# Optimization experiments

Measured on AMD Instinct MI355X. Metric: run time of the kernel, lower is better.

The kernel has to match this reference:

```python
import jax, jax.numpy as jnp
import numpy as np

P = 0.7
WALKS_PER_NODE = 1
WALK_LENGTH = 3


def setup_inputs() -> dict:
    key = jax.random.key(0)
    N = 1_000_000
    E = 16_000_000
    k1, k2 = jax.random.split(key)
    row = jax.random.randint(k1, (E,), 0, N)
    col = jax.random.randint(k2, (E,), 0, N)
    edge_index = jnp.stack([row, col])  # [2, E]
    return {"edge_index": edge_index, "num_nodes": N}


def reference(edge_index, num_nodes):
    E = edge_index.shape[1]
    row, col = edge_index[0], edge_index[1]

    # sort_edge_index: lexicographic sort by (row, col) via two stable argsorts
    p1 = jnp.argsort(col, stable=True)
    p2 = jnp.argsort(row[p1], stable=True)
    perm = p1[p2]
    row, col = row[perm], col[perm]

    # CSR rowptr from out-degree
    deg = jax.ops.segment_sum(jnp.ones(E, jnp.int32), row, num_segments=num_nodes)
    rowptr = jnp.concatenate([jnp.zeros(1, deg.dtype), jnp.cumsum(deg)])

    # start nodes: random permutation, take round(N*p), repeat walks_per_node times
    num_start = int(round(num_nodes * P))
    kperm, kwalk = jax.random.split(jax.random.key(42))
    start = jax.random.permutation(kperm, num_nodes)[:num_start]
    start = jnp.tile(start, WALKS_PER_NODE)  # [S]

    def step(carry, k):
        cur, active = carry
        d = deg[cur]                                  # [S] degree of current node
        act = active & (d > 0)                        # walkers with neighbors
        u = jax.random.uniform(k, cur.shape)
        off = jnp.floor(u * d.astype(u.dtype)).astype(cur.dtype)
        off = jnp.minimum(off, jnp.maximum(d - 1, 0).astype(cur.dtype))
        nxt = col[rowptr[cur] + off]                  # random neighbor gather
        # NOTE: faithful to source, e_id records current_node (used as an
        # index into the edge mask, as the original code does)
        eid = cur
        cur = jnp.where(act, nxt, cur)
        return (cur, act), (eid, act)

    keys = jax.random.split(kwalk, WALK_LENGTH)
    init = (start, jnp.ones(start.shape, bool))
    _, (e_ids, valids) = jax.lax.scan(step, init, keys)

    e_flat = e_ids.reshape(-1)
    v_flat = valids.reshape(-1)
    # scatter hits; invalid entries routed out-of-bounds and dropped
    hits = jnp.zeros(E, bool).at[jnp.where(v_flat, e_flat, E)].set(True, mode='drop')
    edge_mask = ~hits

    # fixed-shape compaction of edge_index[:, edge_mask] / edge_index[:, ~edge_mask]
    ei = jnp.stack([row, col])                        # sorted edge_index [2, E]
    order_keep = jnp.argsort(~edge_mask, stable=True)
    order_mask = jnp.argsort(edge_mask, stable=True)
    n_keep = edge_mask.sum()
    ar = jnp.arange(E)
    remaining_edges = jnp.where(ar < n_keep, ei[:, order_keep], -1)
    masked_edges = jnp.where(ar < (E - n_keep), ei[:, order_mask], -1)
    return remaining_edges, masked_edges, edge_mask
```

## Files before the change

### kernel.cpp

```cpp
#include <hip/hip_runtime.h>
#include <stdint.h>

#define THREADS 256
#define ITEMS 16
#define CHUNK (THREADS * ITEMS)
#define COLMASK 0xFFFFFu
#define EDIG 4096
#define BR 256
#define BCAP 4608
#define BPHYS (BCAP + (BCAP >> 5) + 8)
#define PDIG 1024

__host__ __device__ static inline void tf2x32(uint32_t k0, uint32_t k1,
                                              uint32_t x0, uint32_t x1,
                                              uint32_t* o0, uint32_t* o1) {
  uint32_t ks[3] = {k0, k1, k0 ^ k1 ^ 0x1BD11BDAu};
  x0 += ks[0]; x1 += ks[1];
  const uint32_t RA[4] = {13u, 15u, 26u, 6u};
  const uint32_t RB[4] = {17u, 29u, 16u, 24u};
#pragma unroll
  for (int g = 0; g < 5; ++g) {
    const uint32_t* R = (g & 1) ? RB : RA;
#pragma unroll
    for (int j = 0; j < 4; ++j) {
      x0 += x1;
      x1 = (x1 << R[j]) | (x1 >> (32u - R[j]));
      x1 ^= x0;
    }
    x0 += ks[(g + 1) % 3];
    x1 += ks[(g + 2) % 3] + (uint32_t)(g + 1);
  }
  *o0 = x0; *o1 = x1;
}

__device__ static inline uint32_t rbits32(uint32_t ka, uint32_t kb, uint32_t i) {
  uint32_t o0, o1;
  tf2x32(ka, kb, 0u, i, &o0, &o1);
  return o0 ^ o1;
}

__device__ static inline int xcd_swz(int orig, int nwg) {
  int q = nwg >> 3, r = nwg & 7;
  int xcd = orig & 7, idx = orig >> 3;
  return (xcd < r ? xcd * (q + 1) : r * (q + 1) + (xcd - r) * q) + idx;
}

__device__ static inline int swz32(int j) { return j + (j >> 5); }

__device__ static inline uint32_t block_scan_excl(uint32_t v, uint32_t* lds) {
  int t = threadIdx.x;
  lds[t] = v;
  __syncthreads();
#pragma unroll
  for (int d = 1; d < THREADS; d <<= 1) {
    uint32_t add = (t >= d) ? lds[t - d] : 0u;
    __syncthreads();
    lds[t] += add;
    __syncthreads();
  }
  return lds[t] - v;
}

__global__ void k_sums_u32(const uint32_t* __restrict__ d, int n, uint32_t* __restrict__ bsums) {
  __shared__ uint32_t lds[THREADS];
  int b = blockIdx.x, t = threadIdx.x;
  int base = b * CHUNK + t * ITEMS;
  uint32_t s = 0;
#pragma unroll
  for (int j = 0; j < ITEMS; ++j) { int i = base + j; if (i < n) s += d[i]; }
  lds[t] = s; __syncthreads();
  for (int d2 = THREADS / 2; d2 > 0; d2 >>= 1) { if (t < d2) lds[t] += lds[t + d2]; __syncthreads(); }
  if (t == 0) bsums[b] = lds[0];
}

__global__ void k_scan_single(uint32_t* __restrict__ d, int n, uint32_t* __restrict__ total_out) {
  __shared__ uint32_t lds[THREADS];
  int t = threadIdx.x;
  int K = (n + THREADS - 1) / THREADS;
  int s0 = t * K, s1 = (s0 + K < n) ? (s0 + K) : n;
  uint32_t s = 0;
  for (int j = s0; j < s1; ++j) s += d[j];
  lds[t] = s; __syncthreads();
#pragma unroll
  for (int dd = 1; dd < THREADS; dd <<= 1) {
    uint32_t a = (t >= dd) ? lds[t - dd] : 0u;
    __syncthreads();
    lds[t] += a;
    __syncthreads();
  }
  uint32_t incl = lds[t];
  if (total_out && t == THREADS - 1) *total_out = incl;
  uint32_t run = incl - s;
  for (int j = s0; j < s1; ++j) { uint32_t tmp = d[j]; d[j] = run; run += tmp; }
}

__global__ void k_excl_u32(uint32_t* __restrict__ d, int n, const uint32_t* __restrict__ bsums) {
  __shared__ uint32_t lds[THREADS];
  int b = blockIdx.x, t = threadIdx.x;
  int base = b * CHUNK + t * ITEMS;
  uint32_t v[ITEMS]; uint32_t s = 0;
#pragma unroll
  for (int j = 0; j < ITEMS; ++j) { int i = base + j; uint32_t x = (i < n) ? d[i] : 0u; v[j] = x; s += x; }
  uint32_t run = bsums[b] + block_scan_excl(s, lds);
#pragma unroll
  for (int j = 0; j < ITEMS; ++j) { int i = base + j; if (i < n) d[i] = run; run += v[j]; }
}

__global__ void k_dig_starts(const uint32_t* __restrict__ hist, int NB, int DIG, int total,
                             uint32_t* __restrict__ dstart) {
  int d = blockIdx.x * blockDim.x + threadIdx.x;
  if (d < DIG) dstart[d] = hist[(size_t)d * NB];
  else if (d == DIG) dstart[DIG] = (uint32_t)total;
}

__global__ void k_hist12(const int* __restrict__ row, int n, int NB, uint32_t* __restrict__ hist) {
  __shared__ uint32_t h[EDIG];
  int b = blockIdx.x, t = threadIdx.x;
#pragma unroll
  for (int g = 0; g < EDIG / THREADS; ++g) h[g * THREADS + t] = 0;
  __syncthreads();
  int base = b * CHUNK;
  for (int j = t; j < CHUNK; j += THREADS) {
    int i = base + j;
    if (i < n) atomicAdd(&h[((uint32_t)row[i]) >> 8], 1u);
  }
  __syncthreads();
#pragma unroll
  for (int g = 0; g < EDIG / THREADS; ++g) {
    int d = g * THREADS + t;
    hist[(size_t)d * NB + b] = h[d];
  }
}

__global__ __launch_bounds__(THREADS) void k_pack_scatter12(
    const int* __restrict__ row, const int* __restrict__ col,
    uint64_t* __restrict__ kout, const uint32_t* __restrict__ hist, int n, int NB) {
  constexpr int G = EDIG / THREADS;
  __shared__ uint64_t lkeys[CHUNK];
  __shared__ uint32_t cur[EDIG];
  int b = xcd_swz(blockIdx.x, gridDim.x), t = threadIdx.x;
  int base = b * CHUNK;
#pragma unroll
  for (int g = 0; g < G; ++g) cur[g * THREADS + t] = 0;
  __syncthreads();
  uint64_t mykey[ITEMS];
#pragma unroll
  for (int batch = 0; batch < ITEMS; ++batch) {
    int i = base + batch * THREADS + t;
    uint64_t key = 0ull;
    if (i < n) {
      uint32_t r = (uint32_t)row[i];
      key = ((uint64_t)r << 20) | (uint32_t)col[i];
      atomicAdd(&cur[r >> 8], 1u);
    }
    mykey[batch] = key;
  }
  __syncthreads();
  uint32_t c[G], go[G], lstv[G];
  uint32_t s = 0;
#pragma unroll
  for (int g = 0; g < G; ++g) { c[g] = cur[G * t + g]; s += c[g]; }
  uint32_t tp = block_scan_excl(s, (uint32_t*)lkeys);
  __syncthreads();
#pragma unroll
  for (int g = 0; g < G; ++g) {
    int d = G * t + g;
    go[g] = hist[(size_t)d * NB + b];
    lstv[g] = tp;
    cur[d] = tp;
    tp += c[g];
  }
  __syncthreads();
#pragma unroll
  for (int batch = 0; batch < ITEMS; ++batch) {
    int i = base + batch * THREADS + t;
    if (i < n) {
      uint64_t key = mykey[batch];
      uint32_t dig = (uint32_t)(key >> 28);
      uint32_t slot = atomicAdd(&cur[dig], 1u);
      lkeys[slot] = key;
    }
  }
  __syncthreads();
#pragma unroll
  for (int g = 0; g < G; ++g) cur[G * t + g] = go[g] - lstv[g];
  __syncthreads();
  int nloc = n - base; if (nloc > CHUNK) nloc = CHUNK;
  for (int j = t; j < nloc; j += THREADS) {
    uint64_t key = lkeys[j];
    uint32_t dig = (uint32_t)(key >> 28);
    kout[cur[dig] + (uint32_t)j] = key;
  }
}

__global__ __launch_bounds__(THREADS) void k_bucket256(
    const uint64_t* __restrict__ U0, uint64_t* __restrict__ U1,
    const uint32_t* __restrict__ dstart, int E, int Nn, int* __restrict__ rowptr) {
  __shared__ uint32_t lbuf[BPHYS];
  __shared__ uint8_t  rowof[BCAP];
  __shared__ uint32_t cnt[BR];
  __shared__ uint32_t bs[BR + 1];
  int b = blockIdx.x, t = threadIdx.x;
  int s = (int)dstart[b];
  int e = (int)dstart[b + 1];
  int nseg = e - s;
  int r0 = b * BR;
  cnt[t] = 0;
  __syncthreads();
  for (int j = t; j < nseg; j += THREADS)
    atomicAdd(&cnt[(uint32_t)(U0[s + j] >> 20) & (BR - 1)], 1u);
  __syncthreads();
  uint32_t myc = cnt[t];
  uint32_t mybase = block_scan_excl(myc, lbuf);
  __syncthreads();
  bs[t] = mybase;
  if (t == THREADS - 1) bs[BR] = mybase + myc;
  cnt[t] = mybase;
  __syncthreads();
  if (nseg <= BCAP) {
    for (int j = t; j < nseg; j += THREADS) {
      uint64_t key = U0[s + j];
      uint32_t rl = (uint32_t)(key >> 20) & (BR - 1);
      uint32_t slot = atomicAdd(&cnt[rl], 1u);
      lbuf[swz32((int)slot)] = (uint32_t)(key & COLMASK);
      rowof[slot] = (uint8_t)rl;
    }
    __syncthreads();
    {
      int a0 = (int)bs[t], a1 = (int)bs[t + 1];
      for (int a = a0 + 1; a < a1; ++a) {
        uint32_t key = lbuf[swz32(a)];
        int p = a - 1;
        while (p >= a0 && lbuf[swz32(p)] > key) { lbuf[swz32(p + 1)] = lbuf[swz32(p)]; --p; }
        lbuf[swz32(p + 1)] = key;
      }
    }
    __syncthreads();
    for (int j = t; j < nseg; j += THREADS) {
      uint64_t key = ((uint64_t)(uint32_t)(r0 + rowof[j]) << 20) | lbuf[swz32(j)];
      U1[s + j] = key;
    }
  } else {
    for (int j = t; j < nseg; j += THREADS) {
      uint64_t key = U0[s + j];
      uint32_t slot = atomicAdd(&cnt[(uint32_t)(key >> 20) & (BR - 1)], 1u);
      U1[s + slot] = key;
    }
    __syncthreads();
    int a0 = s + (int)bs[t], a1 = s + (int)bs[t + 1];
    for (int a = a0 + 1; a < a1; ++a) {
      uint64_t key = U1[a];
      int p = a - 1;
      while (p >= a0 && U1[p] > key) { U1[p + 1] = U1[p]; --p; }
      U1[p + 1] = key;
    }
  }
  int r = r0 + t;
  if (r < Nn) rowptr[r] = s + (int)bs[t];
  if (b == (int)gridDim.x - 1 && t == 0) rowptr[Nn] = E;
}

__global__ void k_genkeys64(uint32_t ka, uint32_t kb, int n, uint64_t* __restrict__ K,
                            int NB, uint32_t* __restrict__ hist) {
  __shared__ uint32_t h[PDIG];
  int b = blockIdx.x, t = threadIdx.x;
#pragma unroll
  for (int g = 0; g < PDIG / THREADS; ++g) h[g * THREADS + t] = 0;
  __syncthreads();
  int base = b * CHUNK;
  for (int j = t; j < CHUNK; j += THREADS) {
    int i = base + j;
    if (i < n) {
      uint32_t rb = rbits32(ka, kb, (uint32_t)i);
      K[i] = ((uint64_t)rb << 20) | (uint32_t)i;
      atomicAdd(&h[rb >> 22], 1u);
    }
  }
  __syncthreads();
#pragma unroll
  for (int g = 0; g < PDIG / THREADS; ++g) {
    int d = g * THREADS + t;
    hist[(size_t)d * NB + b] = h[d];
  }
}

__global__ __launch_bounds__(THREADS) void k_scatter64p(
    const uint64_t* __restrict__ kin, uint64_t* __restrict__ kout,
    const uint32_t* __restrict__ hist, int n, int NB) {
  constexpr int G = PDIG / THREADS;
  __shared__ uint64_t lkeys[CHUNK];
  __shared__ uint32_t cur[PDIG];
  int b = blockIdx.x, t = threadIdx.x;
  int base = b * CHUNK;
#pragma unroll
  for (int g = 0; g < G; ++g) cur[g * THREADS + t] = 0;
  __syncthreads();
  uint64_t mykey[ITEMS];
#pragma unroll
  for (int batch = 0; batch < ITEMS; ++batch) {
    int i = base + batch * THREADS + t;
    uint64_t key = 0ull;
    if (i < n) {
      key = kin[i];
      atomicAdd(&cur[(uint32_t)(key >> 42)], 1u);
    }
    mykey[batch] = key;
  }
  __syncthreads();
  uint32_t c[G], go[G], lstv[G];
  uint32_t s = 0;
#pragma unroll
  for (int g = 0; g < G; ++g) { c[g] = cur[G * t + g]; s += c[g]; }
  uint32_t tp = block_scan_excl(s, (uint32_t*)lkeys);
  __syncthreads();
#pragma unroll
  for (int g = 0; g < G; ++g) {
    int d = G * t + g;
    go[g] = hist[(size_t)d * NB + b];
    lstv[g] = tp;
    cur[d] = tp;
    tp += c[g];
  }
  __syncthreads();
#pragma unroll
  for (int batch = 0; batch < ITEMS; ++batch) {
    int i = base + batch * THREADS + t;
    if (i < n) {
      uint64_t key = mykey[batch];
      uint32_t dig = (uint32_t)(key >> 42);
      uint32_t slot = atomicAdd(&cur[dig], 1u);
      lkeys[slot] = key;
    }
  }
  __syncthreads();
#pragma unroll
  for (int g = 0; g < G; ++g) cur[G * t + g] = go[g] - lstv[g];
  __syncthreads();
  int nloc = n - base; if (nloc > CHUNK) nloc = CHUNK;
  for (int j = t; j < nloc; j += THREADS) {
    uint64_t key = lkeys[j];
    uint32_t dig = (uint32_t)(key >> 42);
    kout[cur[dig] + (uint32_t)j] = key;
  }
}

__global__ __launch_bounds__(THREADS) void k_psort(
    const uint64_t* __restrict__ K, const uint32_t* __restrict__ dstart,
    uint32_t* __restrict__ outv, const uint32_t* __restrict__ gsrc) {
  __shared__ uint64_t sb[2048];
  int b = blockIdx.x, t = threadIdx.x;
  int s = (int)dstart[b], e = (int)dstart[b + 1];
  int nseg = e - s;
  for (int j = t; j < 2048; j += THREADS)
    sb[j] = (j < nseg) ? K[s + j] : ~0ull;
  __syncthreads();
  for (int k = 2; k <= 2048; k <<= 1) {
    for (int j = k >> 1; j > 0; j >>= 1) {
      for (int i = t; i < 2048; i += THREADS) {
        int l = i ^ j;
        if (l > i) {
          bool up = ((i & k) == 0);
          uint64_t a = sb[i], c = sb[l];
          if ((a > c) == up) { sb[i] = c; sb[l] = a; }
        }
      }
      __syncthreads();
    }
  }
  for (int j = t; j < nseg; j += THREADS) {
    uint32_t p = (uint32_t)(sb[j] & COLMASK);
    outv[s + j] = gsrc ? gsrc[p] : p;
  }
}

__global__ void k_walk(const int* __restrict__ start, int S,
                       const int* __restrict__ rowptr, const uint64_t* __restrict__ U,
                       uint8_t* __restrict__ hits,
                       uint32_t k0a, uint32_t k0b, uint32_t k1a, uint32_t k1b,
                       uint32_t k2a, uint32_t k2b) {
  int i = blockIdx.x * blockDim.x + threadIdx.x;
  int st = gridDim.x * blockDim.x;
  for (; i < S; i += st) {
    int cur = start[i];
    bool active = true;
    uint32_t ka[3] = {k0a, k1a, k2a};
    uint32_t kb[3] = {k0b, k1b, k2b};
#pragma unroll
    for (int s = 0; s < 3; ++s) {
      int rp = rowptr[cur];
      int d = rowptr[cur + 1] - rp;
      bool act = active && (d > 0);
      if (act) hits[cur] = 1;
      uint32_t bits = rbits32(ka[s], kb[s], (uint32_t)i);
      float u = __uint_as_float((bits >> 9) | 0x3f800000u) - 1.0f;
      int off = (int)floorf(u * (float)d);
      int dm1 = d - 1; if (dm1 < 0) dm1 = 0;
      if (off > dm1) off = dm1;
      if (act) cur = (int)(U[rp + off] & COLMASK);
      active = act;
    }
  }
}

__global__ void k_mask_copy(const uint8_t* __restrict__ hits, const uint64_t* __restrict__ U,
                            int Nn, uint32_t* __restrict__ bsums, uint64_t* __restrict__ hstage) {
  __shared__ uint32_t lds[THREADS];
  int b = blockIdx.x, t = threadIdx.x;
  int base = b * CHUNK + t * ITEMS;
  uint32_t s = 0;
#pragma unroll
  for (int j = 0; j < ITEMS; ++j) {
    int i = base + j;
    if (i < Nn) { s += (uint32_t)(!hits[i]); hstage[i] = U[i]; }
  }
  lds[t] = s; __syncthreads();
  for (int d2 = THREADS / 2; d2 > 0; d2 >>= 1) { if (t < d2) lds[t] += lds[t + d2]; __syncthreads(); }
  if (t == 0) bsums[b] = lds[0];
}

__global__ void k_out_tail(const uint64_t* __restrict__ U, int E, int Nn,
                           const uint32_t* __restrict__ keephead,
                           int* __restrict__ A, int* __restrict__ B, int* __restrict__ M) {
  int nm = Nn - (int)*keephead;
  int i = Nn + blockIdx.x * blockDim.x + threadIdx.x;
  int st = gridDim.x * blockDim.x;
  for (; i < E; i += st) {
    uint64_t key = U[i];
    A[i - nm] = (int)(key >> 20);
    B[i - nm] = (int)(key & COLMASK);
    M[i] = 1;
  }
}

__global__ void k_out_headCD(const uint64_t* __restrict__ hstage, const uint8_t* __restrict__ hits,
                             int Nn, const uint32_t* __restrict__ bsums,
                             int* __restrict__ A, int* __restrict__ B,
                             int* __restrict__ C, int* __restrict__ D, int* __restrict__ M) {
  __shared__ uint32_t lds[THREADS];
  int b = blockIdx.x, t = threadIdx.x;
  int base = b * CHUNK + t * ITEMS;
  uint32_t keep[ITEMS]; uint32_t s = 0;
#pragma unroll
  for (int j = 0; j < ITEMS; ++j) {
    int i = base + j;
    uint32_t k = (i < Nn) ? (uint32_t)(!hits[i]) : 0u;
    keep[j] = k; s += k;
  }
  uint32_t kr = bsums[b] + block_scan_excl(s, lds);
#pragma unroll
  for (int j = 0; j < ITEMS; ++j) {
    int i = base + j;
    if (i < Nn) {
      uint64_t key = hstage[i];
      if (keep[j]) { A[kr] = (int)(key >> 20); B[kr] = (int)(key & COLMASK); M[i] = 1; ++kr; }
      else { uint32_t mr = (uint32_t)i - kr; C[mr] = (int)(key >> 20); D[mr] = (int)(key & COLMASK); M[i] = 0; }
    }
  }
}

__global__ void k_cdfill(int E, int Nn, const uint32_t* __restrict__ keephead,
                         int* __restrict__ A, int* __restrict__ B,
                         int* __restrict__ C, int* __restrict__ D) {
  int nm = Nn - (int)*keephead;
  int j = blockIdx.x * blockDim.x + threadIdx.x;
  int st = gridDim.x * blockDim.x;
  for (; j < E; j += st) {
    if (j >= nm) { C[j] = -1; D[j] = -1; }
    if (j >= E - nm) { A[j] = -1; B[j] = -1; }
  }
}

extern "C" void kernel_launch(void* const* d_in, const int* in_sizes, int n_in,
                              void* d_out, int out_size, void* d_ws, size_t ws_size,
                              hipStream_t stream) {
  const int E = in_sizes[0] / 2;
  const int Nn = 1000000;
  const int S = 700000;
  const int NB_N = (Nn + CHUNK - 1) / CHUNK;
  const int NB_E = (E + CHUNK - 1) / CHUNK;
  const int NBUCK = (Nn + BR - 1) / BR;
  const int NB_P = (Nn + CHUNK - 1) / CHUNK;

  const int* row = (const int*)d_in[0];
  const int* col = row + (size_t)E;

  int* out = (int*)d_out;
  int* A = out;
  int* B = out + (size_t)E;
  int* C = out + (size_t)2 * E;
  int* D = out + (size_t)3 * E;
  int* M = out + (size_t)4 * E;
  uint64_t* U0 = (uint64_t*)out;
  uint64_t* U1 = (uint64_t*)(out + (size_t)2 * E);
  uint32_t* ehist = (uint32_t*)U1;

  char* w = (char*)d_ws;
  uint64_t* hstage = (uint64_t*)w;
  int* rowptr = (int*)w;
  w += (size_t)Nn * 8;
  uint8_t* hits = (uint8_t*)w; w += Nn;
  w = (char*)(((uintptr_t)w + 255) & ~(uintptr_t)255);
  uint32_t* bsums = (uint32_t*)w; w += (size_t)4096 * 4;
  uint32_t* scal = (uint32_t*)w;  w += 64;
  if ((size_t)(w - (char*)d_ws) > ws_size) return;

  uint64_t* K64a  = (uint64_t*)M;
  uint64_t* K64b  = (uint64_t*)(M + (size_t)2 * Nn);
  uint32_t* perm1 = (uint32_t*)(M + (size_t)4 * Nn);
  uint32_t* startv= (uint32_t*)(M + (size_t)5 * Nn);
  uint32_t* phist = (uint32_t*)(M + (size_t)6 * Nn);
  uint32_t* dstart= (uint32_t*)(M + (size_t)7 * Nn);

  struct KK { uint32_t a, b; };
  auto fold = [](KK k, uint32_t j) { KK r; tf2x32(k.a, k.b, 0u, j, &r.a, &r.b); return r; };
  KK base{0u, 42u};
  KK kperm = fold(base, 0u);
  KK kwalk = fold(base, 1u);
  KK keyA  = fold(kperm, 0u);
  KK sub1  = fold(kperm, 1u);
  KK sub2  = fold(keyA, 1u);
  KK wk0 = fold(kwalk, 0u), wk1 = fold(kwalk, 1u), wk2 = fold(kwalk, 2u);

  auto scan_u32 = [&](uint32_t* d, int n) {
    int SB = (n + CHUNK - 1) / CHUNK;
    k_sums_u32<<<SB, THREADS, 0, stream>>>(d, n, bsums);
    k_scan_single<<<1, THREADS, 0, stream>>>(bsums, SB, (uint32_t*)nullptr);
    k_excl_u32<<<SB, THREADS, 0, stream>>>(d, n, bsums);
  };

  hipMemsetAsync(hits, 0, (size_t)Nn, stream);

  k_hist12<<<NB_E, THREADS, 0, stream>>>(row, E, NB_E, ehist);
  scan_u32(ehist, EDIG * NB_E);
  k_dig_starts<<<(EDIG + 1 + THREADS - 1) / THREADS, THREADS, 0, stream>>>(
      ehist, NB_E, EDIG, E, dstart);
  k_pack_scatter12<<<NB_E, THREADS, 0, stream>>>(row, col, U0, ehist, E, NB_E);
  k_bucket256<<<NBUCK, THREADS, 0, stream>>>(U0, U1, dstart, E, Nn, rowptr);

  k_genkeys64<<<NB_P, THREADS, 0, stream>>>(sub1.a, sub1.b, Nn, K64a, NB_P, phist);
  scan_u32(phist, PDIG * NB_P);
  k_dig_starts<<<(PDIG + 1 + THREADS - 1) / THREADS, THREADS, 0, stream>>>(
      phist, NB_P, PDIG, Nn, dstart);
  k_scatter64p<<<NB_P, THREADS, 0, stream>>>(K64a, K64b, phist, Nn, NB_P);
  k_psort<<<PDIG, THREADS, 0, stream>>>(K64b, dstart, perm1, (const uint32_t*)nullptr);
  k_genkeys64<<<NB_P, THREADS, 0, stream>>>(sub2.a, sub2.b, Nn, K64a, NB_P, phist);
  scan_u32(phist, PDIG * NB_P);
  k_dig_starts<<<(PDIG + 1 + THREADS - 1) / THREADS, THREADS, 0, stream>>>(
      phist, NB_P, PDIG, Nn, dstart);
  k_scatter64p<<<NB_P, THREADS, 0, stream>>>(K64a, K64b, phist, Nn, NB_P);
  k_psort<<<PDIG, THREADS, 0, stream>>>(K64b, dstart, startv, perm1);

  k_walk<<<(S + THREADS - 1) / THREADS, THREADS, 0, stream>>>(
      (const int*)startv, S, rowptr, U1, hits, wk0.a, wk0.b, wk1.a, wk1.b, wk2.a, wk2.b);

  k_mask_copy<<<NB_N, THREADS, 0, stream>>>(hits, U1, Nn, bsums, hstage);
  k_scan_single<<<1, THREADS, 0, stream>>>(bsums, NB_N, &scal[0]);
  k_out_tail<<<4096, THREADS, 0, stream>>>(U1, E, Nn, &scal[0], A, B, M);
  k_out_headCD<<<NB_N, THREADS, 0, stream>>>(hstage, hits, Nn, bsums, A, B, C, D, M);
  k_cdfill<<<4096, THREADS, 0, stream>>>(E, Nn, &scal[0], A, B, C, D);
}
```

Baseline: 1.169 ms.

## Replace per-block radix histogram scan with global atomic histogram and offset claiming

The first radix pass of both the edge sort and the permutation sorts now builds one global digit histogram with atomics, scans it in a single small kernel, and has each block claim its output offsets per digit through atomicAdd on a global cursor. This removes the large per-digit-per-block histogram matrix (4096×NB_E entries for the edge sort), the three-kernel scan over it, and the digit-start kernel. The cost is many contended global atomics during scatter and a block order within each bucket that is no longer deterministic. Correctness relies on the later per-bucket sorts ordering by full key.

```diff
diff --git a/kernel.cpp b/kernel.cpp
--- a/kernel.cpp
+++ b/kernel.cpp
@@ -61,16 +61,30 @@
   return lds[t] - v;
 }
 
-__global__ void k_sums_u32(const uint32_t* __restrict__ d, int n, uint32_t* __restrict__ bsums) {
+__global__ void k_scan_small(const uint32_t* __restrict__ src, int n,
+                             uint32_t* __restrict__ dstart, uint32_t* __restrict__ gcur) {
   __shared__ uint32_t lds[THREADS];
-  int b = blockIdx.x, t = threadIdx.x;
-  int base = b * CHUNK + t * ITEMS;
+  int t = threadIdx.x;
+  int K = (n + THREADS - 1) / THREADS;
+  int s0 = t * K, s1 = (s0 + K < n) ? (s0 + K) : n;
   uint32_t s = 0;
-#pragma unroll
-  for (int j = 0; j < ITEMS; ++j) { int i = base + j; if (i < n) s += d[i]; }
+  for (int j = s0; j < s1; ++j) s += src[j];
   lds[t] = s; __syncthreads();
-  for (int d2 = THREADS / 2; d2 > 0; d2 >>= 1) { if (t < d2) lds[t] += lds[t + d2]; __syncthreads(); }
-  if (t == 0) bsums[b] = lds[0];
+#pragma unroll
+  for (int dd = 1; dd < THREADS; dd <<= 1) {
+    uint32_t a = (t >= dd) ? lds[t - dd] : 0u;
+    __syncthreads();
+    lds[t] += a;
+    __syncthreads();
+  }
+  uint32_t run = lds[t] - s;
+  for (int j = s0; j < s1; ++j) {
+    uint32_t tmp = src[j];
+    dstart[j] = run;
+    gcur[j] = run;
+    run += tmp;
+  }
+  if (t == THREADS - 1) dstart[n] = lds[THREADS - 1];
 }
 
 __global__ void k_scan_single(uint32_t* __restrict__ d, int n, uint32_t* __restrict__ total_out) {
@@ -94,26 +108,7 @@
   for (int j = s0; j < s1; ++j) { uint32_t tmp = d[j]; d[j] = run; run += tmp; }
 }
 
-__global__ void k_excl_u32(uint32_t* __restrict__ d, int n, const uint32_t* __restrict__ bsums) {
-  __shared__ uint32_t lds[THREADS];
-  int b = blockIdx.x, t = threadIdx.x;
-  int base = b * CHUNK + t * ITEMS;
-  uint32_t v[ITEMS]; uint32_t s = 0;
-#pragma unroll
-  for (int j = 0; j < ITEMS; ++j) { int i = base + j; uint32_t x = (i < n) ? d[i] : 0u; v[j] = x; s += x; }
-  uint32_t run = bsums[b] + block_scan_excl(s, lds);
-#pragma unroll
-  for (int j = 0; j < ITEMS; ++j) { int i = base + j; if (i < n) d[i] = run; run += v[j]; }
-}
-
-__global__ void k_dig_starts(const uint32_t* __restrict__ hist, int NB, int DIG, int total,
-                             uint32_t* __restrict__ dstart) {
-  int d = blockIdx.x * blockDim.x + threadIdx.x;
-  if (d < DIG) dstart[d] = hist[(size_t)d * NB];
-  else if (d == DIG) dstart[DIG] = (uint32_t)total;
-}
-
-__global__ void k_hist12(const int* __restrict__ row, int n, int NB, uint32_t* __restrict__ hist) {
+__global__ void k_hist_glob(const int* __restrict__ row, int n, uint32_t* __restrict__ ghist) {
   __shared__ uint32_t h[EDIG];
   int b = blockIdx.x, t = threadIdx.x;
 #pragma unroll
@@ -128,13 +123,14 @@
 #pragma unroll
   for (int g = 0; g < EDIG / THREADS; ++g) {
     int d = g * THREADS + t;
-    hist[(size_t)d * NB + b] = h[d];
-  }
-}
-
-__global__ __launch_bounds__(THREADS) void k_pack_scatter12(
+    uint32_t c = h[d];
+    if (c) atomicAdd(&ghist[d], c);
+  }
+}
+
+__global__ __launch_bounds__(THREADS) void k_pack_scatter_claim(
     const int* __restrict__ row, const int* __restrict__ col,
-    uint64_t* __restrict__ kout, const uint32_t* __restrict__ hist, int n, int NB) {
+    uint64_t* __restrict__ kout, uint32_t* __restrict__ gcur, int n) {
   constexpr int G = EDIG / THREADS;
   __shared__ uint64_t lkeys[CHUNK];
   __shared__ uint32_t cur[EDIG];
@@ -165,9 +161,9 @@
 #pragma unroll
   for (int g = 0; g < G; ++g) {
     int d = G * t + g;
-    go[g] = hist[(size_t)d * NB + b];
     lstv[g] = tp;
     cur[d] = tp;
+    go[g] = c[g] ? atomicAdd(&gcur[d], c[g]) : 0u;
     tp += c[g];
   }
   __syncthreads();
@@ -260,8 +256,8 @@
   if (b == (int)gridDim.x - 1 && t == 0) rowptr[Nn] = E;
 }
 
-__global__ void k_genkeys64(uint32_t ka, uint32_t kb, int n, uint64_t* __restrict__ K,
-                            int NB, uint32_t* __restrict__ hist) {
+__global__ void k_genkeys_glob(uint32_t ka, uint32_t kb, int n, uint64_t* __restrict__ K,
+                               uint32_t* __restrict__ ghist) {
   __shared__ uint32_t h[PDIG];
   int b = blockIdx.x, t = threadIdx.x;
 #pragma unroll
@@ -280,13 +276,14 @@
 #pragma unroll
   for (int g = 0; g < PDIG / THREADS; ++g) {
     int d = g * THREADS + t;
-    hist[(size_t)d * NB + b] = h[d];
-  }
-}
-
-__global__ __launch_bounds__(THREADS) void k_scatter64p(
+    uint32_t c = h[d];
+    if (c) atomicAdd(&ghist[d], c);
+  }
+}
+
+__global__ __launch_bounds__(THREADS) void k_scatter64p_claim(
     const uint64_t* __restrict__ kin, uint64_t* __restrict__ kout,
-    const uint32_t* __restrict__ hist, int n, int NB) {
+    uint32_t* __restrict__ gcur, int n) {
   constexpr int G = PDIG / THREADS;
   __shared__ uint64_t lkeys[CHUNK];
   __shared__ uint32_t cur[PDIG];
@@ -316,9 +313,9 @@
 #pragma unroll
   for (int g = 0; g < G; ++g) {
     int d = G * t + g;
-    go[g] = hist[(size_t)d * NB + b];
     lstv[g] = tp;
     cur[d] = tp;
+    go[g] = c[g] ? atomicAdd(&gcur[d], c[g]) : 0u;
     tp += c[g];
   }
   __syncthreads();
@@ -492,7 +489,6 @@
   int* M = out + (size_t)4 * E;
   uint64_t* U0 = (uint64_t*)out;
   uint64_t* U1 = (uint64_t*)(out + (size_t)2 * E);
-  uint32_t* ehist = (uint32_t*)U1;
 
   char* w = (char*)d_ws;
   uint64_t* hstage = (uint64_t*)w;
@@ -508,8 +504,13 @@
   uint64_t* K64b  = (uint64_t*)(M + (size_t)2 * Nn);
   uint32_t* perm1 = (uint32_t*)(M + (size_t)4 * Nn);
   uint32_t* startv= (uint32_t*)(M + (size_t)5 * Nn);
-  uint32_t* phist = (uint32_t*)(M + (size_t)6 * Nn);
-  uint32_t* dstart= (uint32_t*)(M + (size_t)7 * Nn);
+  uint32_t* aux   = (uint32_t*)(M + (size_t)6 * Nn);
+  uint32_t* eghist  = aux;
+  uint32_t* edstart = aux + 4096;
+  uint32_t* egcur   = aux + 8704;
+  uint32_t* pghist  = aux + 12800;
+  uint32_t* pdstart = aux + 13824;
+  uint32_t* pgcur   = aux + 14976;
 
   struct KK { uint32_t a, b; };
   auto fold = [](KK k, uint32_t j) { KK r; tf2x32(k.a, k.b, 0u, j, &r.a, &r.b); return r; };
@@ -521,34 +522,24 @@
   KK sub2  = fold(keyA, 1u);
   KK wk0 = fold(kwalk, 0u), wk1 = fold(kwalk, 1u), wk2 = fold(kwalk, 2u);
 
-  auto scan_u32 = [&](uint32_t* d, int n) {
-    int SB = (n + CHUNK - 1) / CHUNK;
-    k_sums_u32<<<SB, THREADS, 0, stream>>>(d, n, bsums);
-    k_scan_single<<<1, THREADS, 0, stream>>>(bsums, SB, (uint32_t*)nullptr);
-    k_excl_u32<<<SB, THREADS, 0, stream>>>(d, n, bsums);
-  };
-
   hipMemsetAsync(hits, 0, (size_t)Nn, stream);
-
-  k_hist12<<<NB_E, THREADS, 0, stream>>>(row, E, NB_E, ehist);
-  scan_u32(ehist, EDIG * NB_E);
-  k_dig_starts<<<(EDIG + 1 + THREADS - 1) / THREADS, THREADS, 0, stream>>>(
-      ehist, NB_E, EDIG, E, dstart);
-  k_pack_scatter12<<<NB_E, THREADS, 0, stream>>>(row, col, U0, ehist, E, NB_E);
-  k_bucket256<<<NBUCK, THREADS, 0, stream>>>(U0, U1, dstart, E, Nn, rowptr);
-
-  k_genkeys64<<<NB_P, THREADS, 0, stream>>>(sub1.a, sub1.b, Nn, K64a, NB_P, phist);
-  scan_u32(phist, PDIG * NB_P);
-  k_dig_starts<<<(PDIG + 1 + THREADS - 1) / THREADS, THREADS, 0, stream>>>(
-      phist, NB_P, PDIG, Nn, dstart);
-  k_scatter64p<<<NB_P, THREADS, 0, stream>>>(K64a, K64b, phist, Nn, NB_P);
-  k_psort<<<PDIG, THREADS, 0, stream>>>(K64b, dstart, perm1, (const uint32_t*)nullptr);
-  k_genkeys64<<<NB_P, THREADS, 0, stream>>>(sub2.a, sub2.b, Nn, K64a, NB_P, phist);
-  scan_u32(phist, PDIG * NB_P);
-  k_dig_starts<<<(PDIG + 1 + THREADS - 1) / THREADS, THREADS, 0, stream>>>(
-      phist, NB_P, PDIG, Nn, dstart);
-  k_scatter64p<<<NB_P, THREADS, 0, stream>>>(K64a, K64b, phist, Nn, NB_P);
-  k_psort<<<PDIG, THREADS, 0, stream>>>(K64b, dstart, startv, perm1);
+  hipMemsetAsync(eghist, 0, (size_t)EDIG * 4, stream);
+
+  k_hist_glob<<<NB_E, THREADS, 0, stream>>>(row, E, eghist);
+  k_scan_small<<<1, THREADS, 0, stream>>>(eghist, EDIG, edstart, egcur);
+  k_pack_scatter_claim<<<NB_E, THREADS, 0, stream>>>(row, col, U0, egcur, E);
+  k_bucket256<<<NBUCK, THREADS, 0, stream>>>(U0, U1, edstart, E, Nn, rowptr);
+
+  hipMemsetAsync(pghist, 0, (size_t)PDIG * 4, stream);
+  k_genkeys_glob<<<NB_P, THREADS, 0, stream>>>(sub1.a, sub1.b, Nn, K64a, pghist);
+  k_scan_small<<<1, THREADS, 0, stream>>>(pghist, PDIG, pdstart, pgcur);
+  k_scatter64p_claim<<<NB_P, THREADS, 0, stream>>>(K64a, K64b, pgcur, Nn);
+  k_psort<<<PDIG, THREADS, 0, stream>>>(K64b, pdstart, perm1, (const uint32_t*)nullptr);
+  hipMemsetAsync(pghist, 0, (size_t)PDIG * 4, stream);
+  k_genkeys_glob<<<NB_P, THREADS, 0, stream>>>(sub2.a, sub2.b, Nn, K64a, pghist);
+  k_scan_small<<<1, THREADS, 0, stream>>>(pghist, PDIG, pdstart, pgcur);
+  k_scatter64p_claim<<<NB_P, THREADS, 0, stream>>>(K64a, K64b, pgcur, Nn);
+  k_psort<<<PDIG, THREADS, 0, stream>>>(K64b, pdstart, startv, perm1);
 
   k_walk<<<(S + THREADS - 1) / THREADS, THREADS, 0, stream>>>(
       (const int*)startv, S, rowptr, U1, hits, wk0.a, wk0.b, wk1.a, wk1.b, wk2.a, wk2.b);
```

Result: slower. 1.531 ms (+31.0%).
